# Kernel tuning notes

Hardware: AMD Instinct MI355X
Metric: run time of the kernel (lower is better)

Reference implementation:

```python
import jax, jax.numpy as jnp
import numpy as np
import math

N_HEAD = 16
N_EMBED = 1024
BLOCK_SIZE = 2048


def setup_inputs() -> dict:
    key = jax.random.key(0)
    k0, k1, k2, k3, k4 = jax.random.split(key, 5)
    B, T, C = 2, 2048, N_EMBED
    x = jax.random.normal(k0, (B, T, C), dtype=jnp.float32)
    # torch nn.Linear weights: [out_features, in_features]
    s_attn = 1.0 / math.sqrt(C)
    W_attn = jax.random.uniform(k1, (3 * C, C), dtype=jnp.float32, minval=-s_attn, maxval=s_attn)
    b_attn = jax.random.uniform(k2, (3 * C,), dtype=jnp.float32, minval=-s_attn, maxval=s_attn)
    W_proj = jax.random.uniform(k3, (C, C), dtype=jnp.float32, minval=-s_attn, maxval=s_attn)
    b_proj = jax.random.uniform(k4, (C,), dtype=jnp.float32, minval=-s_attn, maxval=s_attn)
    return {"x": x, "W_attn": W_attn, "b_attn": b_attn, "W_proj": W_proj, "b_proj": b_proj}


def reference(x, W_attn, b_attn, W_proj, b_proj):
    B, T, C = x.shape
    H = N_HEAD
    D = C // H
    qkv = x @ W_attn.T + b_attn                     # [B,T,3C]
    q, k, v = jnp.split(qkv, 3, axis=2)
    # [B,T,C] -> [B,H,T,D]
    q = q.reshape(B, T, H, D).transpose(0, 2, 1, 3)
    k = k.reshape(B, T, H, D).transpose(0, 2, 1, 3)
    v = v.reshape(B, T, H, D).transpose(0, 2, 1, 3)
    scale = 1.0 / math.sqrt(D)
    attn = jnp.einsum('bhqd,bhkd->bhqk', q, k) * scale   # [B,H,T,T]
    causal = jnp.tril(jnp.ones((T, T), dtype=bool))
    attn = jnp.where(causal[None, None, :, :], attn, -jnp.inf)
    attn = jax.nn.softmax(attn, axis=-1)
    y = jnp.einsum('bhqk,bhkd->bhqd', attn, v)           # [B,H,T,D]
    y = y.transpose(0, 2, 1, 3).reshape(B, T, C)
    return y @ W_proj.T + b_proj
```

## Files before the change

### kernel.cpp

```cpp
#include <hip/hip_runtime.h>
#include <hip/hip_bf16.h>

#define B_  2
#define T_  2048
#define C_  1024
#define H_  16
#define D_  64
#define M_  (B_*T_)
#define N1_ (3*C_)

typedef short bf16x8 __attribute__((ext_vector_type(8)));
typedef short bf16x4 __attribute__((ext_vector_type(4)));
typedef float f32x4 __attribute__((ext_vector_type(4)));
typedef unsigned short u16;
typedef u16 u16x8 __attribute__((ext_vector_type(8)));

#define QSCALE 0.18033688011112042f
#define C8     11.541560327111707f

__device__ __forceinline__ u16 f2bf(float f) {
  unsigned u = __float_as_uint(f);
  u += 0x7FFFu + ((u >> 16) & 1u);
  return (u16)(u >> 16);
}

__device__ __forceinline__ void gload16(const void* g, void* l) {
  __builtin_amdgcn_global_load_lds((__attribute__((address_space(1))) void*)g,
                                   (__attribute__((address_space(3))) void*)l,
                                   16, 0, 0);
}

__global__ __launch_bounds__(256) void cvt3(const float* __restrict__ x,
                                            const float* __restrict__ wa,
                                            const float* __restrict__ wp,
                                            u16* __restrict__ out) {
  int i = (blockIdx.x * 256 + threadIdx.x) * 8;
  const float* src;
  int off;
  if (i < M_ * C_)                 { src = x;  off = 0; }
  else if (i < M_ * C_ + N1_ * C_) { src = wa; off = M_ * C_; }
  else                             { src = wp; off = M_ * C_ + N1_ * C_; }
  float4 a = *(const float4*)(src + (i - off));
  float4 b = *(const float4*)(src + (i - off) + 4);
  u16x8 o;
  o[0] = f2bf(a.x); o[1] = f2bf(a.y); o[2] = f2bf(a.z); o[3] = f2bf(a.w);
  o[4] = f2bf(b.x); o[5] = f2bf(b.y); o[6] = f2bf(b.z); o[7] = f2bf(b.w);
  *(u16x8*)(out + i) = o;
}

__device__ __forceinline__ void gemm_core(const u16* __restrict__ A,
                                          const u16* __restrict__ W,
                                          u16* As, u16* Bs,
                                          f32x4 (&acc)[4][4],
                                          int m0, int n0, int K) {
  int tid = threadIdx.x;
  int lane = tid & 63, wid = tid >> 6;
  int wr = wid >> 1, wc = wid & 1;

  int arow = wid * 16 + (lane >> 2);
  int ag = lane & 3;
  int sg = ag ^ ((arow >> 1) & 3);
  const u16* aSrc0 = A + (size_t)(m0 + arow) * K + sg * 8;
  const u16* aSrc1 = aSrc0 + (size_t)64 * K;
  const u16* bSrc0 = W + (size_t)(n0 + arow) * K + sg * 8;
  const u16* bSrc1 = bSrc0 + (size_t)64 * K;
  u16* aDst0 = As + (wid * 16) * 32;
  u16* aDst1 = As + (64 + wid * 16) * 32;
  u16* bDst0 = Bs + (wid * 16) * 32;
  u16* bDst1 = Bs + (64 + wid * 16) * 32;

  int rg = lane >> 4;
  int aoff[4], boff[4];
#pragma unroll
  for (int m = 0; m < 4; ++m) {
    int row = wr * 64 + m * 16 + (lane & 15);
    aoff[m] = row * 32 + (rg ^ ((row >> 1) & 3)) * 8;
    row = wc * 64 + m * 16 + (lane & 15);
    boff[m] = row * 32 + (rg ^ ((row >> 1) & 3)) * 8;
  }

  for (int kt = 0; kt < K / 32; ++kt) {
    int k0 = kt * 32;
    __syncthreads();
    gload16(aSrc0 + k0, aDst0);
    gload16(aSrc1 + k0, aDst1);
    gload16(bSrc0 + k0, bDst0);
    gload16(bSrc1 + k0, bDst1);
    __syncthreads();

    bf16x8 af[4], bfr[4];
#pragma unroll
    for (int m = 0; m < 4; ++m) af[m] = *(const bf16x8*)(As + aoff[m]);
#pragma unroll
    for (int n = 0; n < 4; ++n) bfr[n] = *(const bf16x8*)(Bs + boff[n]);
#pragma unroll
    for (int m = 0; m < 4; ++m)
#pragma unroll
      for (int n = 0; n < 4; ++n)
        acc[m][n] = __builtin_amdgcn_mfma_f32_16x16x32_bf16(af[m], bfr[n], acc[m][n], 0, 0, 0);
  }
}

__device__ __forceinline__ void gemm_core64(const u16* __restrict__ A,
                                            const u16* __restrict__ W,
                                            u16* As, u16* Bs,
                                            f32x4 (&acc)[4][2],
                                            int m0, int n0, int K) {
  int tid = threadIdx.x;
  int lane = tid & 63, wid = tid >> 6;
  int wr = wid >> 1, wc = wid & 1;

  int arow = wid * 16 + (lane >> 2);
  int ag = lane & 3;
  int sg = ag ^ ((arow >> 1) & 3);
  const u16* aSrc0 = A + (size_t)(m0 + arow) * K + sg * 8;
  const u16* aSrc1 = aSrc0 + (size_t)64 * K;
  const u16* bSrc  = W + (size_t)(n0 + arow) * K + sg * 8;
  u16* aDst0 = As + (wid * 16) * 32;
  u16* aDst1 = As + (64 + wid * 16) * 32;
  u16* bDst  = Bs + (wid * 16) * 32;

  int rg = lane >> 4;
  int aoff[4], boff[2];
#pragma unroll
  for (int m = 0; m < 4; ++m) {
    int row = wr * 64 + m * 16 + (lane & 15);
    aoff[m] = row * 32 + (rg ^ ((row >> 1) & 3)) * 8;
  }
#pragma unroll
  for (int n = 0; n < 2; ++n) {
    int row = wc * 32 + n * 16 + (lane & 15);
    boff[n] = row * 32 + (rg ^ ((row >> 1) & 3)) * 8;
  }

  for (int kt = 0; kt < K / 32; ++kt) {
    int k0 = kt * 32;
    __syncthreads();
    gload16(aSrc0 + k0, aDst0);
    gload16(aSrc1 + k0, aDst1);
    gload16(bSrc + k0, bDst);
    __syncthreads();

    bf16x8 af[4], bfr[2];
#pragma unroll
    for (int m = 0; m < 4; ++m) af[m] = *(const bf16x8*)(As + aoff[m]);
#pragma unroll
    for (int n = 0; n < 2; ++n) bfr[n] = *(const bf16x8*)(Bs + boff[n]);
#pragma unroll
    for (int m = 0; m < 4; ++m)
#pragma unroll
      for (int n = 0; n < 2; ++n)
        acc[m][n] = __builtin_amdgcn_mfma_f32_16x16x32_bf16(af[m], bfr[n], acc[m][n], 0, 0, 0);
  }
}

__global__ __launch_bounds__(256) void gemm_qkv(const u16* __restrict__ A,
                                                const u16* __restrict__ W,
                                                const float* __restrict__ bias,
                                                u16* __restrict__ Qb,
                                                u16* __restrict__ Kb,
                                                u16* __restrict__ Vt) {
  __shared__ __align__(16) u16 As[128 * 32];
  __shared__ __align__(16) u16 Bs[128 * 32];
  f32x4 acc[4][4] = {};
  int m0 = blockIdx.x * 128, n0 = blockIdx.y * 128;
  gemm_core(A, W, As, Bs, acc, m0, n0, C_);

  int lane = threadIdx.x & 63, wid = threadIdx.x >> 6;
  int wr = wid >> 1, wc = wid & 1;
  int rg = lane >> 4, cl = lane & 15;
#pragma unroll
  for (int n = 0; n < 4; ++n) {
    int gn = n0 + wc * 64 + n * 16 + cl;
    float bv = bias[gn];
    int seg = gn >> 10, cc = gn & 1023;
    int h = cc >> 6, d = cc & 63;
    float sc = (seg == 0) ? QSCALE : 1.0f;
#pragma unroll
    for (int m = 0; m < 4; ++m) {
#pragma unroll
      for (int r = 0; r < 4; ++r) {
        int gm = m0 + wr * 64 + m * 16 + rg * 4 + r;
        int b = gm >> 11, t = gm & 2047;
        u16 val = f2bf((acc[m][n][r] + bv) * sc);
        int bh = b * 16 + h;
        if (seg == 0)      Qb[((size_t)(bh * 2048 + t)) * 64 + d] = val;
        else if (seg == 1) Kb[((size_t)(bh * 2048 + t)) * 64 + d] = val;
        else               Vt[((size_t)(bh * 64 + d)) * 2048 + t] = val;
      }
    }
  }
}

__global__ __launch_bounds__(256) void gemm_proj(const u16* __restrict__ A,
                                                 const u16* __restrict__ W,
                                                 const float* __restrict__ bias,
                                                 float* __restrict__ out) {
  __shared__ __align__(16) u16 As[128 * 32];
  __shared__ __align__(16) u16 Bs[64 * 32];
  f32x4 acc[4][2] = {};
  int m0 = blockIdx.x * 128, n0 = blockIdx.y * 64;
  gemm_core64(A, W, As, Bs, acc, m0, n0, C_);

  int lane = threadIdx.x & 63, wid = threadIdx.x >> 6;
  int wr = wid >> 1, wc = wid & 1;
  int rg = lane >> 4, cl = lane & 15;
#pragma unroll
  for (int n = 0; n < 2; ++n) {
    int gn = n0 + wc * 32 + n * 16 + cl;
    float bv = bias[gn];
#pragma unroll
    for (int m = 0; m < 4; ++m) {
#pragma unroll
      for (int r = 0; r < 4; ++r) {
        int gm = m0 + wr * 64 + m * 16 + rg * 4 + r;
        out[(size_t)gm * 1024 + gn] = acc[m][n][r] + bv;
      }
    }
  }
}

__global__ __launch_bounds__(512, 2) void attn_fwd(const u16* __restrict__ Qb,
                                                   const u16* __restrict__ Kb,
                                                   const u16* __restrict__ Vt,
                                                   u16* __restrict__ Yb) {
  __shared__ __align__(16) u16 Ks[2][64 * 64];
  __shared__ __align__(16) u16 Vs[2][64 * 64];
  __shared__ __align__(16) u16 Ps[8][32 * 32];
  int tid = threadIdx.x, lane = tid & 63, w = tid >> 6;
  int w4 = w >> 1, kvh = w & 1;
  int cl = lane & 15, kg = lane >> 4;
  int sw = (cl ^ (cl >> 2)) & 3;
  int bid = blockIdx.x;
  int bh = bid & 31;
  int i = bid >> 5;
  int qt = (i < 8) ? i : 23 - i;
  int qb0 = qt * 128 + w4 * 32;
  int jmaxw = (qb0 + 31) >> 6;
  int jmaxb = 2 * qt + 1;
  bool hasHigh = (qb0 & 32) != 0;
  const u16* Qp = Qb + (size_t)bh * (2048 * 64);
  const u16* Kp = Kb + (size_t)bh * (2048 * 64);
  const u16* Vp = Vt + (size_t)bh * (64 * 2048);
  u16* Pw = Ps[w];

  int srow8 = lane >> 3;
  int sg = (lane & 7) ^ srow8;
  const u16* Ksrc = Kp + (w * 8 + srow8) * 64 + sg * 8;
  const u16* Vsrc = Vp + (w * 8 + srow8) * 2048 + sg * 8;

  bf16x8 qf[2][2];
#pragma unroll
  for (int fr = 0; fr < 2; ++fr)
#pragma unroll
    for (int dk = 0; dk < 2; ++dk)
      qf[fr][dk] = *(const bf16x8*)(Qp + (qb0 + fr * 16 + cl) * 64 + dk * 32 + kg * 8);

  f32x4 o[2][4] = {};
  float lsum[2] = {0.f, 0.f};
  const f32x4 CINIT = {-C8, -C8, -C8, -C8};

  auto STAGE = [&](int j, int buf) {
    gload16(Ksrc + j * 4096, &Ks[buf][w * 512]);
    gload16(Vsrc + j * 64, &Vs[buf][w * 512]);
  };

  auto CORE = [&](int buf, int j, bool mask) {
    const u16* Kl = Ks[buf];
    const u16* Vl = Vs[buf];
    bf16x8 kf[2][2];
#pragma unroll
    for (int fcl = 0; fcl < 2; ++fcl) {
      int row = (kvh * 2 + fcl) * 16 + cl;
      kf[fcl][0] = *(const bf16x8*)(Kl + row * 64 + ((kg ^ (cl & 7)) * 8));
      kf[fcl][1] = *(const bf16x8*)(Kl + row * 64 + (((4 + kg) ^ (cl & 7)) * 8));
    }
    bf16x8 vf[4];
#pragma unroll
    for (int dc = 0; dc < 4; ++dc) {
      int row = dc * 16 + cl;
      vf[dc] = *(const bf16x8*)(Vl + row * 64 + (((kvh * 4 + kg) ^ (cl & 7)) * 8));
    }
    f32x4 s[2][2];
#pragma unroll
    for (int fcl = 0; fcl < 2; ++fcl)
#pragma unroll
      for (int fr = 0; fr < 2; ++fr) {
        f32x4 z = CINIT;
        z = __builtin_amdgcn_mfma_f32_16x16x32_bf16(kf[fcl][0], qf[fr][0], z, 0, 0, 0);
        z = __builtin_amdgcn_mfma_f32_16x16x32_bf16(kf[fcl][1], qf[fr][1], z, 0, 0, 0);
        s[fr][fcl] = z;
      }
    if (mask) {
#pragma unroll
      for (int fr = 0; fr < 2; ++fr) {
        int qg = qb0 + fr * 16 + cl;
#pragma unroll
        for (int fcl = 0; fcl < 2; ++fcl)
#pragma unroll
          for (int r = 0; r < 4; ++r)
            if (j * 64 + (kvh * 2 + fcl) * 16 + kg * 4 + r > qg) s[fr][fcl][r] = -1e30f;
      }
    }
#pragma unroll
    for (int fr = 0; fr < 2; ++fr) {
      int rowb = (fr * 16 + cl) * 32;
#pragma unroll
      for (int fcl = 0; fcl < 2; ++fcl) {
        float p0 = exp2f(s[fr][fcl][0]);
        float p1 = exp2f(s[fr][fcl][1]);
        float p2 = exp2f(s[fr][fcl][2]);
        float p3 = exp2f(s[fr][fcl][3]);
        lsum[fr] += (p0 + p1) + (p2 + p3);
        union { bf16x4 v; __hip_bfloat162 h[2]; } pk;
        pk.h[0] = __float22bfloat162_rn(make_float2(p0, p1));
        pk.h[1] = __float22bfloat162_rn(make_float2(p2, p3));
        *(bf16x4*)(Pw + rowb + (((fcl * 2 + (kg >> 1)) ^ sw) * 8) + (kg & 1) * 4) = pk.v;
      }
    }
    bf16x8 pf[2];
#pragma unroll
    for (int fr = 0; fr < 2; ++fr)
      pf[fr] = *(const bf16x8*)(Pw + (fr * 16 + cl) * 32 + ((kg ^ sw) * 8));
#pragma unroll
    for (int fr = 0; fr < 2; ++fr)
#pragma unroll
      for (int dc = 0; dc < 4; ++dc)
        o[fr][dc] = __builtin_amdgcn_mfma_f32_16x16x32_bf16(pf[fr], vf[dc], o[fr][dc], 0, 0, 0);
  };

  STAGE(0, 0);
  __syncthreads();
  int buf = 0;
  for (int j = 0; j <= jmaxb; ++j) {
    if (j < jmaxb) STAGE(j + 1, buf ^ 1);
    if (j < jmaxw)       CORE(buf, j, false);
    else if (j == jmaxw && (kvh == 0 || hasHigh)) CORE(buf, j, true);
    __syncthreads();
    buf ^= 1;
  }

  f32x4* Co = (f32x4*)((w4 < 2) ? (void*)&Ks[0][0] : (void*)&Vs[0][0]) + (w4 & 1) * 512;
  float*  Cl = (float*)&Ps[0][0] + w4 * 128;
  if (kvh == 1) {
#pragma unroll
    for (int fr = 0; fr < 2; ++fr) {
      Cl[fr * 64 + lane] = lsum[fr];
#pragma unroll
      for (int dc = 0; dc < 4; ++dc) Co[(fr * 4 + dc) * 64 + lane] = o[fr][dc];
    }
  }
  __syncthreads();
  if (kvh == 0) {
    int b = bh >> 4, h = bh & 15;
#pragma unroll
    for (int fr = 0; fr < 2; ++fr) {
      float l = lsum[fr] + Cl[fr * 64 + lane];
#pragma unroll
      for (int dc = 0; dc < 4; ++dc) o[fr][dc] += Co[(fr * 4 + dc) * 64 + lane];
      l += __shfl_xor(l, 16);
      l += __shfl_xor(l, 32);
      float linv = 1.f / l;
      float li[4];
#pragma unroll
      for (int r = 0; r < 4; ++r) li[r] = __shfl(linv, kg * 4 + r);
#pragma unroll
      for (int dc = 0; dc < 4; ++dc)
#pragma unroll
        for (int r = 0; r < 4; ++r) {
          int t = qb0 + fr * 16 + kg * 4 + r;
          int d = dc * 16 + cl;
          Yb[((size_t)(b * 2048 + t)) * 1024 + h * 64 + d] = f2bf(o[fr][dc][r] * li[r]);
        }
    }
  }
}

extern "C" void kernel_launch(void* const* d_in, const int* in_sizes, int n_in,
                              void* d_out, int out_size, void* d_ws, size_t ws_size,
                              hipStream_t stream) {
  const float* x  = (const float*)d_in[0];
  const float* Wa = (const float*)d_in[1];
  const float* ba = (const float*)d_in[2];
  const float* Wp = (const float*)d_in[3];
  const float* bp = (const float*)d_in[4];
  float* out = (float*)d_out;

  u16* xb  = (u16*)d_ws;
  u16* Wab = xb  + (size_t)M_ * C_;
  u16* Wpb = Wab + (size_t)N1_ * C_;
  u16* Qb  = Wpb + (size_t)C_ * C_;
  u16* Kb  = Qb  + (size_t)M_ * C_;
  u16* Vt  = Kb  + (size_t)M_ * C_;
  u16* Yb  = Vt  + (size_t)M_ * C_;

  cvt3<<<(M_ * C_ + N1_ * C_ + C_ * C_) / 2048, 256, 0, stream>>>(x, Wa, Wp, xb);
  gemm_qkv<<<dim3(M_ / 128, N1_ / 128), 256, 0, stream>>>(xb, Wab, ba, Qb, Kb, Vt);
  attn_fwd<<<512, 512, 0, stream>>>(Qb, Kb, Vt, Yb);
  gemm_proj<<<dim3(M_ / 128, C_ / 64), 256, 0, stream>>>(Yb, Wpb, bp, out);
}
```

Before: 110.3 us.

## Split QKV GEMM K-loop across two wave groups with LDS reduction

The QKV projection GEMM now runs 512 threads per block, split into two groups of four waves. Each group handles alternating 32-wide K slices into its own LDS buffer, and the two partial accumulators are then summed through shared memory before the epilogue. The aim is more waves in flight per block to hide load latency and halve the number of serial K iterations. In exchange it adds an LDS reduction with extra barriers and doubles shared memory per block, which may reduce occupancy.

```diff
diff --git a/kernel.cpp b/kernel.cpp
--- a/kernel.cpp
+++ b/kernel.cpp
@@ -48,26 +48,32 @@
   *(u16x8*)(out + i) = o;
 }
 
-__device__ __forceinline__ void gemm_core(const u16* __restrict__ A,
-                                          const u16* __restrict__ W,
-                                          u16* As, u16* Bs,
-                                          f32x4 (&acc)[4][4],
-                                          int m0, int n0, int K) {
+__global__ __launch_bounds__(512) void gemm_qkv(const u16* __restrict__ A,
+                                                const u16* __restrict__ W,
+                                                const float* __restrict__ bias,
+                                                u16* __restrict__ Qb,
+                                                u16* __restrict__ Kb,
+                                                u16* __restrict__ Vt) {
+  __shared__ __align__(16) u16 As[2][128 * 32];
+  __shared__ __align__(16) u16 Bs[2][128 * 32];
+  const int K = C_;
   int tid = threadIdx.x;
   int lane = tid & 63, wid = tid >> 6;
-  int wr = wid >> 1, wc = wid & 1;
-
-  int arow = wid * 16 + (lane >> 2);
+  int wg = wid >> 2, w4 = wid & 3;
+  int wr = w4 >> 1, wc = w4 & 1;
+  int m0 = blockIdx.x * 128, n0 = blockIdx.y * 128;
+
+  int arow = w4 * 16 + (lane >> 2);
   int ag = lane & 3;
   int sg = ag ^ ((arow >> 1) & 3);
-  const u16* aSrc0 = A + (size_t)(m0 + arow) * K + sg * 8;
+  const u16* aSrc0 = A + (size_t)(m0 + arow) * K + wg * 32 + sg * 8;
   const u16* aSrc1 = aSrc0 + (size_t)64 * K;
-  const u16* bSrc0 = W + (size_t)(n0 + arow) * K + sg * 8;
+  const u16* bSrc0 = W + (size_t)(n0 + arow) * K + wg * 32 + sg * 8;
   const u16* bSrc1 = bSrc0 + (size_t)64 * K;
-  u16* aDst0 = As + (wid * 16) * 32;
-  u16* aDst1 = As + (64 + wid * 16) * 32;
-  u16* bDst0 = Bs + (wid * 16) * 32;
-  u16* bDst1 = Bs + (64 + wid * 16) * 32;
+  u16* aDst0 = &As[wg][(w4 * 16) * 32];
+  u16* aDst1 = &As[wg][(64 + w4 * 16) * 32];
+  u16* bDst0 = &Bs[wg][(w4 * 16) * 32];
+  u16* bDst1 = &Bs[wg][(64 + w4 * 16) * 32];
 
   int rg = lane >> 4;
   int aoff[4], boff[4];
@@ -79,8 +85,9 @@
     boff[m] = row * 32 + (rg ^ ((row >> 1) & 3)) * 8;
   }
 
-  for (int kt = 0; kt < K / 32; ++kt) {
-    int k0 = kt * 32;
+  f32x4 acc[4][4] = {};
+  for (int kt = 0; kt < K / 64; ++kt) {
+    int k0 = kt * 64;
     __syncthreads();
     gload16(aSrc0 + k0, aDst0);
     gload16(aSrc1 + k0, aDst1);
@@ -90,14 +97,60 @@
 
     bf16x8 af[4], bfr[4];
 #pragma unroll
-    for (int m = 0; m < 4; ++m) af[m] = *(const bf16x8*)(As + aoff[m]);
-#pragma unroll
-    for (int n = 0; n < 4; ++n) bfr[n] = *(const bf16x8*)(Bs + boff[n]);
+    for (int m = 0; m < 4; ++m) af[m] = *(const bf16x8*)(&As[wg][0] + aoff[m]);
+#pragma unroll
+    for (int n = 0; n < 4; ++n) bfr[n] = *(const bf16x8*)(&Bs[wg][0] + boff[n]);
 #pragma unroll
     for (int m = 0; m < 4; ++m)
 #pragma unroll
       for (int n = 0; n < 4; ++n)
         acc[m][n] = __builtin_amdgcn_mfma_f32_16x16x32_bf16(af[m], bfr[n], acc[m][n], 0, 0, 0);
+  }
+
+  f32x4* Sc = (f32x4*)&As[0][0];
+  __syncthreads();
+#pragma unroll
+  for (int p = 0; p < 2; ++p) {
+    if (wg == 1 && wr == p) {
+#pragma unroll
+      for (int m = 0; m < 4; ++m)
+#pragma unroll
+        for (int n = 0; n < 4; ++n)
+          Sc[(wc * 64 + lane) * 16 + m * 4 + n] = acc[m][n];
+    }
+    __syncthreads();
+    if (wg == 0 && wr == p) {
+#pragma unroll
+      for (int m = 0; m < 4; ++m)
+#pragma unroll
+        for (int n = 0; n < 4; ++n)
+          acc[m][n] += Sc[(wc * 64 + lane) * 16 + m * 4 + n];
+    }
+    __syncthreads();
+  }
+
+  if (wg != 0) return;
+  int cl = lane & 15;
+#pragma unroll
+  for (int n = 0; n < 4; ++n) {
+    int gn = n0 + wc * 64 + n * 16 + cl;
+    float bv = bias[gn];
+    int seg = gn >> 10, cc = gn & 1023;
+    int h = cc >> 6, d = cc & 63;
+    float sc2 = (seg == 0) ? QSCALE : 1.0f;
+#pragma unroll
+    for (int m = 0; m < 4; ++m) {
+#pragma unroll
+      for (int r = 0; r < 4; ++r) {
+        int gm = m0 + wr * 64 + m * 16 + rg * 4 + r;
+        int b = gm >> 11, t = gm & 2047;
+        u16 val = f2bf((acc[m][n][r] + bv) * sc2);
+        int bh = b * 16 + h;
+        if (seg == 0)      Qb[((size_t)(bh * 2048 + t)) * 64 + d] = val;
+        else if (seg == 1) Kb[((size_t)(bh * 2048 + t)) * 64 + d] = val;
+        else               Vt[((size_t)(bh * 64 + d)) * 2048 + t] = val;
+      }
+    }
   }
 }
 
@@ -151,44 +204,6 @@
 #pragma unroll
       for (int n = 0; n < 2; ++n)
         acc[m][n] = __builtin_amdgcn_mfma_f32_16x16x32_bf16(af[m], bfr[n], acc[m][n], 0, 0, 0);
-  }
-}
-
-__global__ __launch_bounds__(256) void gemm_qkv(const u16* __restrict__ A,
-                                                const u16* __restrict__ W,
-                                                const float* __restrict__ bias,
-                                                u16* __restrict__ Qb,
-                                                u16* __restrict__ Kb,
-                                                u16* __restrict__ Vt) {
-  __shared__ __align__(16) u16 As[128 * 32];
-  __shared__ __align__(16) u16 Bs[128 * 32];
-  f32x4 acc[4][4] = {};
-  int m0 = blockIdx.x * 128, n0 = blockIdx.y * 128;
-  gemm_core(A, W, As, Bs, acc, m0, n0, C_);
-
-  int lane = threadIdx.x & 63, wid = threadIdx.x >> 6;
-  int wr = wid >> 1, wc = wid & 1;
-  int rg = lane >> 4, cl = lane & 15;
-#pragma unroll
-  for (int n = 0; n < 4; ++n) {
-    int gn = n0 + wc * 64 + n * 16 + cl;
-    float bv = bias[gn];
-    int seg = gn >> 10, cc = gn & 1023;
-    int h = cc >> 6, d = cc & 63;
-    float sc = (seg == 0) ? QSCALE : 1.0f;
-#pragma unroll
-    for (int m = 0; m < 4; ++m) {
-#pragma unroll
-      for (int r = 0; r < 4; ++r) {
-        int gm = m0 + wr * 64 + m * 16 + rg * 4 + r;
-        int b = gm >> 11, t = gm & 2047;
-        u16 val = f2bf((acc[m][n][r] + bv) * sc);
-        int bh = b * 16 + h;
-        if (seg == 0)      Qb[((size_t)(bh * 2048 + t)) * 64 + d] = val;
-        else if (seg == 1) Kb[((size_t)(bh * 2048 + t)) * 64 + d] = val;
-        else               Vt[((size_t)(bh * 64 + d)) * 2048 + t] = val;
-      }
-    }
   }
 }
 
@@ -395,7 +410,7 @@
   u16* Yb  = Vt  + (size_t)M_ * C_;
 
   cvt3<<<(M_ * C_ + N1_ * C_ + C_ * C_) / 2048, 256, 0, stream>>>(x, Wa, Wp, xb);
-  gemm_qkv<<<dim3(M_ / 128, N1_ / 128), 256, 0, stream>>>(xb, Wab, ba, Qb, Kb, Vt);
+  gemm_qkv<<<dim3(M_ / 128, N1_ / 128), 512, 0, stream>>>(xb, Wab, ba, Qb, Kb, Vt);
   attn_fwd<<<512, 512, 0, stream>>>(Qb, Kb, Vt, Yb);
   gemm_proj<<<dim3(M_ / 128, C_ / 64), 256, 0, stream>>>(Yb, Wpb, bp, out);
 }
```

Result: slower. 126.2 us (+14.4%).
